# Kernel optimization log

Measured on AMD Instinct MI355X. Metric: run time of the kernel, lower is better.

Reference implementation:

```python
import jax, jax.numpy as jnp
from jax import lax
import numpy as np

B, T, I, H = 4096, 200, 32, 6  # batch, seq_len, input_size, hidden


def _lstm_layer(x_seq, W_ih, W_hh, b_ih, b_hh):
    """Single unidirectional LSTM layer, PyTorch gate order (i,f,g,o).
    x_seq: [B,T,Din]. Returns (all_h [B,T,H], h_last [B,H])."""
    Bb = x_seq.shape[0]
    Hh = W_hh.shape[1]
    # Precompute input projections for all timesteps (hoisted out of the scan).
    x_proj = jnp.einsum('bti,gi->btg', x_seq, W_ih) + b_ih + b_hh  # [B,T,4H]

    def step(carry, xp_t):
        h, c = carry
        gates = xp_t + h @ W_hh.T  # [B,4H]
        i_g, f_g, g_g, o_g = jnp.split(gates, 4, axis=-1)
        i_g = jax.nn.sigmoid(i_g)
        f_g = jax.nn.sigmoid(f_g)
        g_g = jnp.tanh(g_g)
        o_g = jax.nn.sigmoid(o_g)
        c = f_g * c + i_g * g_g
        h = o_g * jnp.tanh(c)
        return (h, c), h

    init = (jnp.zeros((Bb, Hh), x_seq.dtype), jnp.zeros((Bb, Hh), x_seq.dtype))
    (h_last, _), hs = lax.scan(step, init, jnp.swapaxes(x_proj, 0, 1))  # time-major scan
    return jnp.swapaxes(hs, 0, 1), h_last


def setup_inputs() -> dict:
    key = jax.random.key(0)
    ks = jax.random.split(key, 11)
    s = 0.2  # ~ uniform(-1/sqrt(H)) scale for H=6
    inp = {
        'x': jax.random.normal(ks[0], (B, T, I), dtype=jnp.float32),
        'W_ih0': jax.random.normal(ks[1], (4 * H, I), dtype=jnp.float32) * s,
        'W_hh0': jax.random.normal(ks[2], (4 * H, H), dtype=jnp.float32) * s,
        'b_ih0': jax.random.normal(ks[3], (4 * H,), dtype=jnp.float32) * s,
        'b_hh0': jax.random.normal(ks[4], (4 * H,), dtype=jnp.float32) * s,
        'W_ih1': jax.random.normal(ks[5], (4 * H, H), dtype=jnp.float32) * s,
        'W_hh1': jax.random.normal(ks[6], (4 * H, H), dtype=jnp.float32) * s,
        'b_ih1': jax.random.normal(ks[7], (4 * H,), dtype=jnp.float32) * s,
        'b_hh1': jax.random.normal(ks[8], (4 * H,), dtype=jnp.float32) * s,
        'W_lin': jax.random.normal(ks[9], (1, H), dtype=jnp.float32) * s,
        'b_lin': jax.random.normal(ks[10], (1,), dtype=jnp.float32) * s,
    }
    return inp


def reference(x, W_ih0, W_hh0, b_ih0, b_hh0, W_ih1, W_hh1, b_ih1, b_hh1, W_lin, b_lin):
    # Layer 0 (eval mode: inter-layer dropout disabled)
    h1_seq, _ = _lstm_layer(x, W_ih0, W_hh0, b_ih0, b_hh0)
    # Layer 1
    _, h2_last = _lstm_layer(h1_seq, W_ih1, W_hh1, b_ih1, b_hh1)
    # Linear head on last layer's final hidden state: [B,1]
    return h2_last @ W_lin.T + b_lin
```

## Files before the change

kernel.cpp:

```cpp
#include <hip/hip_runtime.h>


#define TLEN  200
#define ISZ   32
#define HSZ   6
#define WPITCH 36

#define RPITCH 25
#define RING_DW (64 * RPITCH)
#define FWOFF  RING_DW
#define FBOFF  (FWOFF + 24 * WPITCH)
#define FLDS_DW (FBOFF + 24)

#define XP4_COUNT ((size_t)4096 * TLEN * 6)
#define WS_REQ    ((XP4_COUNT + 6) * 16)

__device__ __forceinline__ float fast_sig(float x) {
    return __builtin_amdgcn_rcpf(1.0f + __expf(-x));
}
__device__ __forceinline__ float tanh_s(float x) {
    return fmaf(2.0f, fast_sig(x + x), -1.0f);
}
__device__ __forceinline__ float rl(float v, int l) {
    return __int_as_float(__builtin_amdgcn_readlane(__float_as_int(v), l));
}
template <int CTRL>
__device__ __forceinline__ float qperm(float v) {
    return __int_as_float(__builtin_amdgcn_mov_dpp(__float_as_int(v), CTRL, 0xf, 0xf, true));
}
template <int OFF>
__device__ __forceinline__ float swz(float v) {
    return __int_as_float(__builtin_amdgcn_ds_swizzle(__float_as_int(v), OFF));
}
__device__ __forceinline__ float dot4(float4 w, float4 v) {
    return fmaf(w.x, v.x, fmaf(w.y, v.y, fmaf(w.z, v.z, w.w * v.w)));
}

__global__ __launch_bounds__(64) void proj_k3(
    const float* __restrict__ x,    const float* __restrict__ Wih0,
    const float* __restrict__ bih0, const float* __restrict__ bhh0,
    const float* __restrict__ bih1, const float* __restrict__ bhh1,
    float4* __restrict__ xp4)
{
    __shared__ float xs[64 * 36];

    const int lane = threadIdx.x;
    const int b    = blockIdx.x;
    const float* xb = x + (size_t)b * TLEN * ISZ;

    if (b == 0 && lane < 24) {
        const int u = lane % 6, g = lane / 6;
        ((float*)(xp4 + XP4_COUNT))[u * 4 + g] = bih1[g * 6 + u] + bhh1[g * 6 + u];
    }

    const int s  = lane / 24;
    const int se = (s == 2) ? 0 : s;
    const int g  = lane - s * 24;
    const bool act = (lane < 48);

    float4 w4[8];
    const float4* wr = (const float4*)(Wih0 + g * ISZ);
#pragma unroll
    for (int q = 0; q < 8; ++q) w4[q] = wr[q];
    const float bg = bih0[g] + bhh0[g];

    const int ofs = (g % 6) * 4 + g / 6;
    float* xpb = (float*)(xp4 + (size_t)b * TLEN * 6);

#pragma unroll 1
    for (int tc = 0; tc < TLEN; tc += 64) {
        const int nrows = (TLEN - tc >= 64) ? 64 : (TLEN - tc);
        const float4* src = (const float4*)(xb + (size_t)tc * ISZ);
        for (int f = lane; f < nrows * 8; f += 64) {
            const int row = f >> 3, kq = f & 7;
            *(float4*)&xs[row * 36 + kq * 4] = src[f];
        }
        const int half = nrows >> 1;
#pragma unroll 1
        for (int i = 0; i < half; ++i) {
            const int rr = 2 * i + se;
            float a0 = bg, a1 = 0.0f;
#pragma unroll
            for (int q = 0; q < 4; ++q) {
                const float4 xv = *(const float4*)&xs[rr * 36 + q * 4];
                a0 = fmaf(w4[q].x, xv.x, a0); a0 = fmaf(w4[q].y, xv.y, a0);
                a0 = fmaf(w4[q].z, xv.z, a0); a0 = fmaf(w4[q].w, xv.w, a0);
            }
#pragma unroll
            for (int q = 4; q < 8; ++q) {
                const float4 xv = *(const float4*)&xs[rr * 36 + q * 4];
                a1 = fmaf(w4[q].x, xv.x, a1); a1 = fmaf(w4[q].y, xv.y, a1);
                a1 = fmaf(w4[q].z, xv.z, a1); a1 = fmaf(w4[q].w, xv.w, a1);
            }
            const float a = a0 + a1;
            if (act) xpb[(size_t)(tc + rr) * 24 + ofs] = a;
        }
    }
}

__global__ __launch_bounds__(64) void scan_k4(
    const float* __restrict__ Whh0, const float* __restrict__ Wih1,
    const float* __restrict__ Whh1, const float* __restrict__ Wlin,
    const float* __restrict__ blin, const float4* __restrict__ xp4,
    float* __restrict__ out)
{
    const int lane = threadIdx.x;
    const int role = lane & 15;
    const int grp  = lane >> 4;
    const bool act = (grp < 2);
    const int b    = blockIdx.x * 2 + (grp & 1);

    float WA[4][6], WB[4][6];
#pragma unroll
    for (int gg = 0; gg < 4; ++gg)
#pragma unroll
        for (int k = 0; k < 6; ++k) { WA[gg][k] = 0.0f; WB[gg][k] = 0.0f; }
    if (act && role < 6) {
#pragma unroll
        for (int gg = 0; gg < 4; ++gg)
#pragma unroll
            for (int k = 0; k < 6; ++k) WA[gg][k] = Whh0[(gg * 6 + role) * 6 + k];
    } else if (act && role < 12) {
        const int u = role - 6;
#pragma unroll
        for (int gg = 0; gg < 4; ++gg)
#pragma unroll
            for (int k = 0; k < 6; ++k) {
                WA[gg][k] = Wih1[(gg * 6 + u) * 6 + k];
                WB[gg][k] = Whh1[(gg * 6 + u) * 6 + k];
            }
    }

    const float4* P;
    int ST;
    if (act && role < 6) { P = xp4 + (size_t)b * TLEN * 6 + role; ST = 6; }
    else { P = xp4 + XP4_COUNT + ((role >= 6 && role < 12) ? role - 6 : 0); ST = 0; }

    float4 q0 = P[0], q1 = P[ST], q2 = P[2 * ST], q3 = P[3 * ST];
    P += 4 * ST;

    float c = 0.0f, h = 0.0f;

#define ARG(A, G) do { \
    const float s0 = fmaf(WA[G][0], hA0, fmaf(WA[G][1], hA1, fmaf(WA[G][2], hA2, A))); \
    const float s1 = fmaf(WA[G][3], hA3, fmaf(WA[G][4], hA4, WA[G][5] * hA5)); \
    const float s2 = fmaf(WB[G][0], hB0, fmaf(WB[G][1], hB1, WB[G][2] * hB2)); \
    const float s3 = fmaf(WB[G][3], hB3, fmaf(WB[G][4], hB4, WB[G][5] * hB5)); \
    A = (s0 + s1) + (s2 + s3); \
} while (0)

#define STEP(XQ) do { \
    const float hA0 = swz<0x010>(h), hA1 = swz<0x030>(h), hA2 = swz<0x050>(h); \
    const float hA3 = swz<0x070>(h), hA4 = swz<0x090>(h), hA5 = swz<0x0B0>(h); \
    const float hB0 = swz<0x0D0>(h), hB1 = swz<0x0F0>(h), hB2 = swz<0x110>(h); \
    const float hB3 = swz<0x130>(h), hB4 = swz<0x150>(h), hB5 = swz<0x170>(h); \
    float a0 = (XQ).x, a1 = (XQ).y, a2 = (XQ).z, a3 = (XQ).w; \
    ARG(a0, 0); ARG(a1, 1); ARG(a2, 2); ARG(a3, 3); \
    const float ig = fast_sig(a0), fg = fast_sig(a1); \
    const float gg = tanh_s(a2),   og = fast_sig(a3); \
    c = fmaf(fg, c, ig * gg); \
    h = og * tanh_s(c); \
} while (0)

#define STEPR(QV) do { const float4 _xq = QV; QV = *P; P += ST; STEP(_xq); } while (0)

    STEPR(q0);
    h = (role < 6) ? h : 0.0f;
    c = (role < 6) ? c : 0.0f;

#pragma unroll 1
    for (int m = 0; m < 48; ++m) {
        STEPR(q1); STEPR(q2); STEPR(q3); STEPR(q0);
    }
    STEPR(q1); STEPR(q2); STEPR(q3);
    STEP(q0); STEP(q1); STEP(q2); STEP(q3);
    STEP(q0);

    {
        const float f0 = swz<0x0D0>(h), f1 = swz<0x0F0>(h), f2 = swz<0x110>(h);
        const float f3 = swz<0x130>(h), f4 = swz<0x150>(h), f5 = swz<0x170>(h);
        float sOut = blin[0];
        sOut = fmaf(Wlin[0], f0, sOut); sOut = fmaf(Wlin[1], f1, sOut);
        sOut = fmaf(Wlin[2], f2, sOut); sOut = fmaf(Wlin[3], f3, sOut);
        sOut = fmaf(Wlin[4], f4, sOut); sOut = fmaf(Wlin[5], f5, sOut);
        if (act && role == 0) out[b] = sOut;
    }
#undef STEP
#undef STEPR
#undef ARG
}

__global__ __launch_bounds__(64) void lstm_fb(
    const float* __restrict__ x,
    const float* __restrict__ Wih0, const float* __restrict__ Whh0,
    const float* __restrict__ bih0, const float* __restrict__ bhh0,
    const float* __restrict__ Wih1, const float* __restrict__ Whh1,
    const float* __restrict__ bih1, const float* __restrict__ bhh1,
    const float* __restrict__ Wlin, const float* __restrict__ blin,
    float* __restrict__ out)
{
    __shared__ float lds[FLDS_DW];

    const int lane = threadIdx.x;
    const int b    = blockIdx.x;

    const int o = lane & 1;
    const int L = lane >> 1;

    const bool loHalf = (lane < 32);
    const int  p  = lane & 3;
    const int  jq = (lane & 31) >> 2;
    const int  j  = (jq < HSZ) ? jq : 0;
    const int  r  = 6 * p + j;

#define LDSW(ROW, KCQ) (*(const float4*)&lds[FWOFF + (o * 12 + (ROW)) * WPITCH + ((KCQ) << 2)])

#pragma unroll
    for (int k = 0; k < 13; ++k) {
        const int idx = lane + (k << 6);
        if (idx < 768) {
            const int row = idx >> 5, kk = idx & 31;
            lds[FWOFF + row * WPITCH + kk] = Wih0[idx];
        } else if (idx < 792) {
            lds[FBOFF + idx - 768] = bih0[idx - 768] + bhh0[idx - 768];
        }
    }

    float WA[6], WB[6], base1 = 0.0f, sgc = 1.0f, tgc = 0.0f;
#pragma unroll
    for (int k = 0; k < 6; ++k) { WA[k] = 0.0f; WB[k] = 0.0f; }
    if (loHalf) {
#pragma unroll
        for (int k = 0; k < 6; ++k) WA[k] = Whh0[r * 6 + k];
    } else {
#pragma unroll
        for (int k = 0; k < 6; ++k) { WA[k] = Wih1[r * 6 + k]; WB[k] = Whh1[r * 6 + k]; }
        base1 = bih1[r] + bhh1[r];
    }
    if (p == 2) {
#pragma unroll
        for (int k = 0; k < 6; ++k) { WA[k] *= 2.0f; WB[k] *= 2.0f; }
        base1 *= 2.0f; sgc = 2.0f; tgc = -1.0f;
    }

    const float* xb = x + (size_t)b * TLEN * ISZ;

#pragma unroll
    for (int w01 = 0; w01 < 2; ++w01) {
        const int t = (w01 << 5) + L;
        const float4* xr4 = (const float4*)(xb + t * ISZ);
        float4 xw[8];
#pragma unroll
        for (int q = 0; q < 8; ++q) xw[q] = xr4[q];
        float a0c[12];
#pragma unroll
        for (int jj = 0; jj < 12; ++jj) a0c[jj] = 0.0f;
#pragma unroll
        for (int kc = 0; kc < 8; ++kc)
#pragma unroll
            for (int jj = 0; jj < 12; ++jj)
                a0c[jj] += dot4(LDSW(jj, kc), xw[kc]);
#pragma unroll
        for (int jj = 0; jj < 12; ++jj) {
            float v = a0c[jj] + lds[FBOFF + o * 12 + jj];
            if (jj < 6) v = (o == 1) ? v * 2.0f : v;
            lds[t * RPITCH + o * 12 + jj] = v;
        }
    }

    float acc[12];
#pragma unroll
    for (int jj = 0; jj < 12; ++jj) acc[jj] = 0.0f;
    const float* pc = xb + (size_t)min(64 + L, TLEN - 1) * ISZ;
    const float* pn = xb + (size_t)min(96 + L, TLEN - 1) * ISZ;
    float4 f0, f1;
    f1 = *((const float4*)pc);
    float4 Wp0 = LDSW(0, 0), Wp1 = LDSW(1, 0), Wp2 = LDSW(2, 0);

    float c = 0.0f, h = 0.0f;
    float xp_cur = lds[r];

#define KC_HEAD(KC) do { \
    f0 = f1; \
    const float4* _srcp = ((KC) < 7) ? ((const float4*)pc + (KC) + 1) \
                                     : ((const float4*)pn); \
    f1 = *_srcp; \
} while (0)

#define SPREAD_STEP(RT, KC) do { \
    acc[3*(RT)+0] += dot4(Wp0, f0); \
    acc[3*(RT)+1] += dot4(Wp1, f0); \
    acc[3*(RT)+2] += dot4(Wp2, f0); \
    const int _rtn = ((RT) + 1) & 3; \
    const int _kcn = ((RT) == 3) ? (((KC) + 1) & 7) : (KC); \
    Wp0 = LDSW(3*_rtn + 0, _kcn); \
    Wp1 = LDSW(3*_rtn + 1, _kcn); \
    Wp2 = LDSW(3*_rtn + 2, _kcn); \
} while (0)

#define SCAN_STEP(ITV) do { \
    const float h10=rl(h,0),  h11=rl(h,4),  h12=rl(h,8); \
    const float h13=rl(h,12), h14=rl(h,16), h15=rl(h,20); \
    const float h20=rl(h,32), h21=rl(h,36), h22=rl(h,40); \
    const float h23=rl(h,44), h24=rl(h,48), h25=rl(h,52); \
    const float _xn = lds[(((ITV) + 1) & 63) * RPITCH + r]; \
    const float _g0 = loHalf ? xp_cur : base1; \
    const float _a0 = fmaf(WA[0],h10, fmaf(WA[2],h12, fmaf(WA[4],h14, _g0))); \
    const float _a1 = fmaf(WA[1],h11, fmaf(WA[3],h13, WA[5]*h15)); \
    const float _b0 = fmaf(WB[0],h20, fmaf(WB[2],h22, WB[4]*h24)); \
    const float _b1 = fmaf(WB[1],h21, fmaf(WB[3],h23, WB[5]*h25)); \
    const float _g  = (_a0 + _a1) + (_b0 + _b1); \
    const float _aG = fmaf(sgc, fast_sig(_g), tgc); \
    const float _iq = qperm<0x00>(_aG), _fq = qperm<0x55>(_aG); \
    const float _gq = qperm<0xAA>(_aG), _oq = qperm<0xFF>(_aG); \
    c = fmaf(_fq, c, _iq * _gq); \
    const float _th = fmaf(2.0f, fast_sig(2.0f * c), -1.0f); \
    h = _oq * _th; \
    xp_cur = _xn; \
    if ((ITV) == 200) { \
        float _s = blin[0]; \
        _s = fmaf(Wlin[0], rl(h, 32), _s); \
        _s = fmaf(Wlin[1], rl(h, 36), _s); \
        _s = fmaf(Wlin[2], rl(h, 40), _s); \
        _s = fmaf(Wlin[3], rl(h, 44), _s); \
        _s = fmaf(Wlin[4], rl(h, 48), _s); \
        _s = fmaf(Wlin[5], rl(h, 52), _s); \
        if (lane == 0) out[b] = _s; \
    } \
} while (0)

#define ENTRY(IT0) do { \
    const int _slot = ((IT0) + 32 + L) & 63; \
    _Pragma("unroll") \
    for (int _jj = 0; _jj < 12; ++_jj) { \
        float _v = acc[_jj] + lds[FBOFF + o * 12 + _jj]; \
        if (_jj < 6) _v = (o == 1) ? _v * 2.0f : _v; \
        lds[_slot * RPITCH + o * 12 + _jj] = _v; \
        acc[_jj] = 0.0f; \
    } \
    pc = pn; \
    pn = xb + (size_t)min((IT0) + 96 + L, TLEN - 1) * ISZ; \
} while (0)

    KC_HEAD(0);
    SPREAD_STEP(0, 0);
    {
        const float g  = loHalf ? xp_cur : base1;
        const float aG = fmaf(sgc, fast_sig(g), tgc);
        const float iq = qperm<0x00>(aG), gq = qperm<0xAA>(aG), oq = qperm<0xFF>(aG);
        const float cn = iq * gq;
        const float th = fmaf(2.0f, fast_sig(2.0f * cn), -1.0f);
        c = loHalf ? cn : 0.0f;
        h = loHalf ? (oq * th) : 0.0f;
        xp_cur = lds[RPITCH + r];
    }

    SPREAD_STEP(1, 0); SCAN_STEP(1);
    SPREAD_STEP(2, 0); SCAN_STEP(2);
    SPREAD_STEP(3, 0); SCAN_STEP(3);
    for (int kc = 1; kc < 8; ++kc) {
        KC_HEAD(kc);
        const int itb = kc << 2;
        SPREAD_STEP(0, kc); SCAN_STEP(itb + 0);
        SPREAD_STEP(1, kc); SCAN_STEP(itb + 1);
        SPREAD_STEP(2, kc); SCAN_STEP(itb + 2);
        SPREAD_STEP(3, kc); SCAN_STEP(itb + 3);
    }

    for (int w = 1; w < 7; ++w) {
        const int it0 = w << 5;
        ENTRY(it0);
        for (int kc = 0; kc < 8; ++kc) {
            const int itb = it0 + (kc << 2);
            if (itb > 200) break;
            KC_HEAD(kc);
            SPREAD_STEP(0, kc); SCAN_STEP(itb + 0);
            SPREAD_STEP(1, kc); SCAN_STEP(itb + 1);
            SPREAD_STEP(2, kc); SCAN_STEP(itb + 2);
            SPREAD_STEP(3, kc); SCAN_STEP(itb + 3);
        }
    }

#undef LDSW
#undef KC_HEAD
#undef SPREAD_STEP
#undef SCAN_STEP
#undef ENTRY
}

extern "C" void kernel_launch(void* const* d_in, const int* in_sizes, int n_in,
                              void* d_out, int out_size, void* d_ws, size_t ws_size,
                              hipStream_t stream) {
    const float* x    = (const float*)d_in[0];
    const float* Wih0 = (const float*)d_in[1];
    const float* Whh0 = (const float*)d_in[2];
    const float* bih0 = (const float*)d_in[3];
    const float* bhh0 = (const float*)d_in[4];
    const float* Wih1 = (const float*)d_in[5];
    const float* Whh1 = (const float*)d_in[6];
    const float* bih1 = (const float*)d_in[7];
    const float* bhh1 = (const float*)d_in[8];
    const float* Wlin = (const float*)d_in[9];
    const float* blin = (const float*)d_in[10];
    float* out = (float*)d_out;

    if (d_ws != nullptr && ws_size >= WS_REQ) {
        float4* xp4 = (float4*)d_ws;
        proj_k3<<<4096, 64, 0, stream>>>(x, Wih0, bih0, bhh0, bih1, bhh1, xp4);
        scan_k4<<<2048, 64, 0, stream>>>(Whh0, Wih1, Whh1, Wlin, blin,
                                         (const float4*)xp4, out);
    } else {
        lstm_fb<<<4096, 64, 0, stream>>>(x, Wih0, Whh0, bih0, bhh0,
                                         Wih1, Whh1, bih1, bhh1,
                                         Wlin, blin, out);
    }
}
```

Baseline: 274.3 us.

## Stream projection inputs through registers and pack four sequences per scan wave

The projection kernel no longer stages x rows in LDS. Each lane group now loads its row of x directly into registers, double-buffered so the next row's load is in flight while the current row is computed, which removes the LDS round trip and the barrier-free copy loop. The scan kernel now uses all four 16-lane groups of a wave for four independent sequences instead of two, halving the grid to 1024 blocks. The trade-off is higher register pressure from the double buffer, redundant per-lane global loads of the same row, and fewer waves available to hide latency in the scan.

Result: slower. 374.0 us (+36.3%).

```diff
diff --git a/kernel.cpp b/kernel.cpp
--- a/kernel.cpp
+++ b/kernel.cpp
@@ -36,26 +36,22 @@
     return fmaf(w.x, v.x, fmaf(w.y, v.y, fmaf(w.z, v.z, w.w * v.w)));
 }
 
-__global__ __launch_bounds__(64) void proj_k3(
+__global__ __launch_bounds__(64) void proj_v5(
     const float* __restrict__ x,    const float* __restrict__ Wih0,
     const float* __restrict__ bih0, const float* __restrict__ bhh0,
     const float* __restrict__ bih1, const float* __restrict__ bhh1,
     float4* __restrict__ xp4)
 {
-    __shared__ float xs[64 * 36];
-
     const int lane = threadIdx.x;
     const int b    = blockIdx.x;
-    const float* xb = x + (size_t)b * TLEN * ISZ;
 
     if (b == 0 && lane < 24) {
         const int u = lane % 6, g = lane / 6;
         ((float*)(xp4 + XP4_COUNT))[u * 4 + g] = bih1[g * 6 + u] + bhh1[g * 6 + u];
     }
 
-    const int s  = lane / 24;
-    const int se = (s == 2) ? 0 : s;
-    const int g  = lane - s * 24;
+    const int  par = (lane >= 24 && lane < 48) ? 1 : 0;
+    const int  g   = (lane < 24) ? lane : (lane < 48 ? lane - 24 : lane - 48);
     const bool act = (lane < 48);
 
     float4 w4[8];
@@ -64,41 +60,47 @@
     for (int q = 0; q < 8; ++q) w4[q] = wr[q];
     const float bg = bih0[g] + bhh0[g];
 
+    const float* xr = x + (size_t)b * TLEN * ISZ + par * ISZ;
+    float* xpb = (float*)(xp4 + (size_t)b * TLEN * 6);
     const int ofs = (g % 6) * 4 + g / 6;
-    float* xpb = (float*)(xp4 + (size_t)b * TLEN * 6);
+
+    float4 A[8], B[8];
+#pragma unroll
+    for (int q = 0; q < 8; ++q) A[q] = ((const float4*)xr)[q];
+#pragma unroll
+    for (int q = 0; q < 8; ++q) B[q] = ((const float4*)(xr + 64))[q];
+
+#define PCOMP(BUF, R) do { \
+    float a0 = bg, a1 = 0.0f; \
+    _Pragma("unroll") \
+    for (int q = 0; q < 4; ++q) { \
+        a0 = fmaf(w4[q].x, BUF[q].x, a0); a0 = fmaf(w4[q].y, BUF[q].y, a0); \
+        a0 = fmaf(w4[q].z, BUF[q].z, a0); a0 = fmaf(w4[q].w, BUF[q].w, a0); \
+    } \
+    _Pragma("unroll") \
+    for (int q = 4; q < 8; ++q) { \
+        a1 = fmaf(w4[q].x, BUF[q].x, a1); a1 = fmaf(w4[q].y, BUF[q].y, a1); \
+        a1 = fmaf(w4[q].z, BUF[q].z, a1); a1 = fmaf(w4[q].w, BUF[q].w, a1); \
+    } \
+    const float a = a0 + a1; \
+    if (act) xpb[(size_t)(2 * (R) + par) * 24 + ofs] = a; \
+} while (0)
 
 #pragma unroll 1
-    for (int tc = 0; tc < TLEN; tc += 64) {
-        const int nrows = (TLEN - tc >= 64) ? 64 : (TLEN - tc);
-        const float4* src = (const float4*)(xb + (size_t)tc * ISZ);
-        for (int f = lane; f < nrows * 8; f += 64) {
-            const int row = f >> 3, kq = f & 7;
-            *(float4*)&xs[row * 36 + kq * 4] = src[f];
-        }
-        const int half = nrows >> 1;
-#pragma unroll 1
-        for (int i = 0; i < half; ++i) {
-            const int rr = 2 * i + se;
-            float a0 = bg, a1 = 0.0f;
-#pragma unroll
-            for (int q = 0; q < 4; ++q) {
-                const float4 xv = *(const float4*)&xs[rr * 36 + q * 4];
-                a0 = fmaf(w4[q].x, xv.x, a0); a0 = fmaf(w4[q].y, xv.y, a0);
-                a0 = fmaf(w4[q].z, xv.z, a0); a0 = fmaf(w4[q].w, xv.w, a0);
-            }
-#pragma unroll
-            for (int q = 4; q < 8; ++q) {
-                const float4 xv = *(const float4*)&xs[rr * 36 + q * 4];
-                a1 = fmaf(w4[q].x, xv.x, a1); a1 = fmaf(w4[q].y, xv.y, a1);
-                a1 = fmaf(w4[q].z, xv.z, a1); a1 = fmaf(w4[q].w, xv.w, a1);
-            }
-            const float a = a0 + a1;
-            if (act) xpb[(size_t)(tc + rr) * 24 + ofs] = a;
-        }
-    }
-}
-
-__global__ __launch_bounds__(64) void scan_k4(
+    for (int k = 0; k < 49; ++k) {
+        PCOMP(A, 2 * k);
+#pragma unroll
+        for (int q = 0; q < 8; ++q) A[q] = ((const float4*)(xr + (2 * k + 2) * 64))[q];
+        PCOMP(B, 2 * k + 1);
+#pragma unroll
+        for (int q = 0; q < 8; ++q) B[q] = ((const float4*)(xr + (2 * k + 3) * 64))[q];
+    }
+    PCOMP(A, 98);
+    PCOMP(B, 99);
+#undef PCOMP
+}
+
+__global__ __launch_bounds__(64) void scan_k5(
     const float* __restrict__ Whh0, const float* __restrict__ Wih1,
     const float* __restrict__ Whh1, const float* __restrict__ Wlin,
     const float* __restrict__ blin, const float4* __restrict__ xp4,
@@ -107,20 +109,19 @@
     const int lane = threadIdx.x;
     const int role = lane & 15;
     const int grp  = lane >> 4;
-    const bool act = (grp < 2);
-    const int b    = blockIdx.x * 2 + (grp & 1);
+    const int b    = blockIdx.x * 4 + grp;
 
     float WA[4][6], WB[4][6];
 #pragma unroll
     for (int gg = 0; gg < 4; ++gg)
 #pragma unroll
         for (int k = 0; k < 6; ++k) { WA[gg][k] = 0.0f; WB[gg][k] = 0.0f; }
-    if (act && role < 6) {
+    if (role < 6) {
 #pragma unroll
         for (int gg = 0; gg < 4; ++gg)
 #pragma unroll
             for (int k = 0; k < 6; ++k) WA[gg][k] = Whh0[(gg * 6 + role) * 6 + k];
-    } else if (act && role < 12) {
+    } else if (role < 12) {
         const int u = role - 6;
 #pragma unroll
         for (int gg = 0; gg < 4; ++gg)
@@ -133,8 +134,8 @@
 
     const float4* P;
     int ST;
-    if (act && role < 6) { P = xp4 + (size_t)b * TLEN * 6 + role; ST = 6; }
-    else { P = xp4 + XP4_COUNT + ((role >= 6 && role < 12) ? role - 6 : 0); ST = 0; }
+    if (role < 6) { P = xp4 + (size_t)b * TLEN * 6 + role; ST = 6; }
+    else          { P = xp4 + XP4_COUNT + (role < 12 ? role - 6 : 0); ST = 0; }
 
     float4 q0 = P[0], q1 = P[ST], q2 = P[2 * ST], q3 = P[3 * ST];
     P += 4 * ST;
@@ -183,7 +184,7 @@
         sOut = fmaf(Wlin[0], f0, sOut); sOut = fmaf(Wlin[1], f1, sOut);
         sOut = fmaf(Wlin[2], f2, sOut); sOut = fmaf(Wlin[3], f3, sOut);
         sOut = fmaf(Wlin[4], f4, sOut); sOut = fmaf(Wlin[5], f5, sOut);
-        if (act && role == 0) out[b] = sOut;
+        if (role == 0) out[b] = sOut;
     }
 #undef STEP
 #undef STEPR
@@ -406,8 +407,8 @@
 
     if (d_ws != nullptr && ws_size >= WS_REQ) {
         float4* xp4 = (float4*)d_ws;
-        proj_k3<<<4096, 64, 0, stream>>>(x, Wih0, bih0, bhh0, bih1, bhh1, xp4);
-        scan_k4<<<2048, 64, 0, stream>>>(Whh0, Wih1, Whh1, Wlin, blin,
+        proj_v5<<<4096, 64, 0, stream>>>(x, Wih0, bih0, bhh0, bih1, bhh1, xp4);
+        scan_k5<<<1024, 64, 0, stream>>>(Whh0, Wih1, Whh1, Wlin, blin,
                                          (const float4*)xp4, out);
     } else {
         lstm_fb<<<4096, 64, 0, stream>>>(x, Wih0, Whh0, bih0, bhh0,
```
